# Kernel optimization log

Measured on AMD Instinct MI355X. Metric: run time of the kernel, lower is better.

The kernel has to match this reference:

```python
import jax, jax.numpy as jnp
import numpy as np

PATCH = 3  # match_patch_size

def _to_patches(fm, nph, npw):
    # fm: [1, C, H, W] -> [nph*npw, C*PATCH*PATCH] non-overlapping 3x3 patches
    C = fm.shape[1]
    x = fm[0, :, :nph * PATCH, :npw * PATCH].reshape(C, nph, PATCH, npw, PATCH)
    x = x.transpose(1, 3, 0, 2, 4)  # [nph, npw, C, p, p]
    return x.reshape(nph * npw, C * PATCH * PATCH)

def _from_patches(p, nph, npw, C):
    # [nph*npw, C*p*p] -> [1, C, nph*p, npw*p]
    x = p.reshape(nph, npw, C, PATCH, PATCH).transpose(2, 0, 3, 1, 4)
    return x.reshape(1, C, nph * PATCH, npw * PATCH)

def setup_inputs() -> dict:
    key = jax.random.key(0)
    k1, k2, k3 = jax.random.split(key, 3)
    C, H, W = 512, 252, 252
    style_fm = jax.random.normal(k1, (1, C, H, W), dtype=jnp.float32)
    img_fm = jax.random.normal(k2, (1, C, H, W), dtype=jnp.float32)
    mask = jax.random.uniform(k3, (1, 1, H, W), dtype=jnp.float32)
    return {"style_fm": style_fm, "img_fm": img_fm, "mask": mask}

def reference(style_fm, img_fm, mask):
    B, C, H, W = style_fm.shape  # B == 1
    nph, npw = H // PATCH, W // PATCH
    # Patch match: each img patch is a conv kernel applied to style_fm with
    # stride=PATCH -> score positions == non-overlapping style patch grid.
    img_p = _to_patches(img_fm, nph, npw)      # [P, D]
    sty_p = _to_patches(style_fm, nph, npw)    # [Q, D]
    scores = img_p @ sty_p.T                   # [P, Q] cross-correlation
    idx = jnp.argmax(scores, axis=1)           # best style patch per img patch
    matched = sty_p[idx]                       # [P, D] gather
    matched_fm = _from_patches(matched, nph, npw, C)
    style_matched = style_fm.at[:, :, :nph * PATCH, :npw * PATCH].set(matched_fm)
    # Mask (expanded as in capture_content), then Gram / sum(expanded mask)
    masked = style_matched * mask
    mask_sum = jnp.sum(jnp.broadcast_to(mask, style_matched.shape))
    gram = jnp.einsum('bchw,bdhw->bcd', masked, masked) / mask_sum  # [1, C, C]
    return gram
```

## Files before the change

### kernel.cpp

```cpp
#include <hip/hip_runtime.h>
#include <stdint.h>

typedef _Float16 f16;
typedef _Float16 f16x8 __attribute__((ext_vector_type(8)));
typedef float f32x4 __attribute__((ext_vector_type(4)));

#define NCH   512
#define IMH   252
#define IMW   252
#define HWSZ  (IMH*IMW)
#define NP    84
#define PN    (NP*NP)
#define PPAD  7168
#define DD    (NCH*9)
#define KK2   (PPAD*9)
#define KSPLIT 48
#define KCH   (KK2/KSPLIT)
#define MARGIN 1.0f

#define AS1(p) ((const __attribute__((address_space(1))) void*)(p))
#define AS3(p) ((__attribute__((address_space(3))) void*)(p))

__global__ void k_init(f16* __restrict__ I, f16* __restrict__ S,
                       int* cnt, float* msum) {
  unsigned t = blockIdx.x * blockDim.x + threadIdx.x;
  if (t == 0) { *cnt = 0; *msum = 0.0f; }
  const unsigned padN = (PPAD - PN) * DD;
  for (unsigned i = t; i < padN; i += gridDim.x * blockDim.x) {
    I[(size_t)PN * DD + i] = (f16)0.0f;
    S[(size_t)PN * DD + i] = (f16)0.0f;
  }
}

__global__ void k_masksum(const float* __restrict__ mask, float* msum) {
  __shared__ float red[256];
  float s = 0.f;
  for (unsigned i = blockIdx.x * 256 + threadIdx.x; i < HWSZ; i += gridDim.x * 256)
    s += mask[i];
  red[threadIdx.x] = s; __syncthreads();
  for (int st = 128; st > 0; st >>= 1) {
    if ((int)threadIdx.x < st) red[threadIdx.x] += red[threadIdx.x + st];
    __syncthreads();
  }
  if (threadIdx.x == 0) atomicAdd(msum, red[0]);
}

__global__ __launch_bounds__(256)
void k_pack(const float* __restrict__ fm, f16* __restrict__ out) {
  __shared__ f16 T[32 * 756];
  const int py = blockIdx.x >> 4, cg = blockIdx.x & 15;
  const int c0 = cg * 32;
  for (int e = threadIdx.x; e < 32 * 756; e += 256) {
    int cc = e / 756, rx = e - cc * 756;
    T[e] = (f16)fm[(size_t)(c0 + cc) * HWSZ +
                   (size_t)(py * 3 + rx / 252) * IMW + (rx % 252)];
  }
  __syncthreads();
  for (int v = threadIdx.x; v < 84 * 36; v += 256) {
    int pxi = v / 36, d0 = (v - pxi * 36) * 8;
    f16x8 o;
#pragma unroll
    for (int k = 0; k < 8; ++k) {
      int d = d0 + k, cc = d / 9, j = d - cc * 9;
      o[k] = T[cc * 756 + (j / 3) * 252 + pxi * 3 + (j % 3)];
    }
    *(f16x8*)(out + (size_t)(py * NP + pxi) * DD + c0 * 9 + d0) = o;
  }
}

__global__ __launch_bounds__(512, 2)
void k_gemm256(const f16* __restrict__ A, const f16* __restrict__ B,
               f16* __restrict__ out) {
  __shared__ f16 Al[4][256][32];
  __shared__ f16 Bl[4][256][32];
  const int tid = threadIdx.x, w = tid >> 6, l = tid & 63;
  int bid = blockIdx.x;
  bid = (bid & 7) * 98 + (bid >> 3);
  const int bx = bid % 28, by = bid / 28;
  const size_t row0 = (size_t)by * 256, col0 = (size_t)bx * 256;
  const int wm = w >> 2, wn = w & 3;
  f32x4 acc[8][4] = {};
  const int srow = w * 16 + (l >> 2);
  const int scol = (l & 3) * 8;
  const f16* gA0 = A + (row0 + srow) * DD + scol;
  const f16* gA1 = A + (row0 + srow + 128) * DD + scol;
  const f16* gB0 = B + (col0 + srow) * DD + scol;
  const f16* gB1 = B + (col0 + srow + 128) * DD + scol;
  const int ldst = w * 512 + l * 8;
#define STG(tt, bb) do {                                                        \
    __builtin_amdgcn_global_load_lds(AS1(gA0 + (tt)*32), AS3(&Al[bb][0][0] + ldst),        16, 0, 0); \
    __builtin_amdgcn_global_load_lds(AS1(gA1 + (tt)*32), AS3(&Al[bb][0][0] + 4096 + ldst), 16, 0, 0); \
    __builtin_amdgcn_global_load_lds(AS1(gB0 + (tt)*32), AS3(&Bl[bb][0][0] + ldst),        16, 0, 0); \
    __builtin_amdgcn_global_load_lds(AS1(gB1 + (tt)*32), AS3(&Bl[bb][0][0] + 4096 + ldst), 16, 0, 0); \
  } while (0)
  STG(0, 0); STG(1, 1); STG(2, 2);
  const int fr = l & 15, kb = (l >> 4) * 8;
  const int NT = DD / 32;
  for (int t = 0; t < NT; ++t) {
    const int ts = (t + 3 < NT) ? t + 3 : NT - 1;
    const int bb = t & 3;
    STG(ts, (t + 3) & 3);
    asm volatile("s_waitcnt vmcnt(12)" ::: "memory");
    __builtin_amdgcn_s_barrier();
    __builtin_amdgcn_sched_barrier(0);
    f16x8 af[8], bf[4];
#pragma unroll
    for (int i = 0; i < 8; ++i) af[i] = *(const f16x8*)&Al[bb][wm * 128 + i * 16 + fr][kb];
#pragma unroll
    for (int j = 0; j < 4; ++j) bf[j] = *(const f16x8*)&Bl[bb][wn * 64 + j * 16 + fr][kb];
#pragma unroll
    for (int i = 0; i < 8; ++i)
#pragma unroll
      for (int j = 0; j < 4; ++j)
        acc[i][j] = __builtin_amdgcn_mfma_f32_16x16x32_f16(af[i], bf[j], acc[i][j], 0, 0, 0);
    asm volatile("s_waitcnt lgkmcnt(0)" ::: "memory");
    __builtin_amdgcn_sched_barrier(0);
    __builtin_amdgcn_s_barrier();
  }
#undef STG
  const int fq = l >> 4;
  const size_t orow = row0 + wm * 128, ocol = col0 + wn * 64;
#pragma unroll
  for (int i = 0; i < 8; ++i)
#pragma unroll
    for (int j = 0; j < 4; ++j)
#pragma unroll
      for (int r = 0; r < 4; ++r)
        out[(orow + i * 16 + fq * 4 + r) * PPAD + (ocol + j * 16 + fr)] =
            (f16)acc[i][j][r];
}

__global__ void k_top2(const f16* __restrict__ sc, int* __restrict__ idx,
                       float* __restrict__ max1v, int* __restrict__ amb, int* cnt) {
  const int p = blockIdx.x;
  const f16x8* row8 = (const f16x8*)(sc + (size_t)p * PPAD);
  float m1 = -1e30f, m2 = -1e30f; int i1 = 0;
  for (int v = threadIdx.x; v < PN / 8; v += 256) {
    f16x8 x = row8[v];
#pragma unroll
    for (int k = 0; k < 8; ++k) {
      float val = (float)x[k];
      if (val > m1) { m2 = m1; m1 = val; i1 = v * 8 + k; }
      else if (val > m2) m2 = val;
    }
  }
  __shared__ float sm1[256], sm2[256]; __shared__ int si1[256];
  const int t = threadIdx.x;
  sm1[t] = m1; sm2[t] = m2; si1[t] = i1; __syncthreads();
  for (int st = 128; st > 0; st >>= 1) {
    if (t < st) {
      float am1 = sm1[t], am2 = sm2[t]; int ai1 = si1[t];
      float bm1 = sm1[t + st], bm2 = sm2[t + st]; int bi1 = si1[t + st];
      if (bm1 > am1 || (bm1 == am1 && bi1 < ai1)) {
        sm1[t] = bm1; si1[t] = bi1; sm2[t] = fmaxf(am1, bm2);
      } else {
        sm2[t] = fmaxf(bm1, am2);
      }
    }
    __syncthreads();
  }
  if (t == 0) {
    idx[p] = si1[0]; max1v[p] = sm1[0];
    if (sm2[0] > sm1[0] - MARGIN) { int a = atomicAdd(cnt, 1); amb[a] = p; }
  }
}

__global__ void k_rescore(const float* __restrict__ img, const float* __restrict__ sty,
                          const f16* __restrict__ sc, const float* __restrict__ max1v,
                          const int* __restrict__ amb, const int* __restrict__ cnt,
                          int* __restrict__ idx) {
  __shared__ float red[256];
  __shared__ unsigned long long ball[4];
  const int t = threadIdx.x;
  const int n = *cnt;
  for (int r = blockIdx.x; r < n; r += gridDim.x) {
    const int p = amb[r];
    const float thr = max1v[p] - MARGIN;
    const f16* row = sc + (size_t)p * PPAD;
    const int py = (p / NP) * 3, px = (p % NP) * 3;
    float best = -1e30f; int bq = 0x7fffffff;
    for (int base = 0; base < PN; base += 256) {
      const int q = base + t;
      const bool is_cand = (q < PN) && ((float)row[q] >= thr);
      unsigned long long m = __ballot(is_cand);
      if ((t & 63) == 0) ball[t >> 6] = m;
      __syncthreads();
      for (int wv = 0; wv < 4; ++wv) {
        unsigned long long mm = ball[wv];
        while (mm) {
          const int b = __ffsll(mm) - 1; mm &= mm - 1;
          const int q2 = base + wv * 64 + b;
          const int qy = (q2 / NP) * 3, qx = (q2 % NP) * 3;
          float s = 0.f;
          for (int d = t; d < DD; d += 256) {
            int c = d / 9, j = d - c * 9, dy = j / 3, dx = j - dy * 3;
            s += img[(size_t)c * HWSZ + (py + dy) * IMW + (px + dx)] *
                 sty[(size_t)c * HWSZ + (qy + dy) * IMW + (qx + dx)];
          }
          red[t] = s; __syncthreads();
          for (int st = 128; st > 0; st >>= 1) {
            if (t < st) red[t] += red[t + st];
            __syncthreads();
          }
          const float tot = red[0];
          __syncthreads();
          if (tot > best || (tot == best && q2 < bq)) { best = tot; bq = q2; }
        }
      }
      __syncthreads();
    }
    if (t == 0) idx[p] = bq;
    __syncthreads();
  }
}

__global__ __launch_bounds__(256)
void k_masked(const f16* __restrict__ S, const int* __restrict__ idx,
              const float* __restrict__ mask, f16* __restrict__ M) {
  __shared__ f16 B[84 * 288];
  __shared__ float mrow[756];
  __shared__ int qv[84];
  const int py = blockIdx.x >> 4, cg = blockIdx.x & 15;
  const int c0 = cg * 32;
  for (int e = threadIdx.x; e < 756; e += 256)
    mrow[e] = mask[(size_t)(py * 3 + e / 252) * IMW + (e % 252)];
  if (threadIdx.x < 84) qv[threadIdx.x] = idx[py * NP + threadIdx.x];
  __syncthreads();
  for (int v = threadIdx.x; v < 84 * 36; v += 256) {
    int pxi = v / 36, d0 = (v - pxi * 36) * 8;
    f16x8 x = *(const f16x8*)(S + (size_t)qv[pxi] * DD + c0 * 9 + d0);
    f16x8 o;
#pragma unroll
    for (int k = 0; k < 8; ++k) {
      int j = (d0 + k) % 9;
      o[k] = (f16)((float)x[k] * mrow[(j / 3) * 252 + pxi * 3 + (j % 3)]);
    }
    *(f16x8*)(&B[pxi * 288 + d0]) = o;
  }
  __syncthreads();
  for (int e = threadIdx.x; e < 32 * 756; e += 256) {
    int cc = e / 756, r = e - cc * 756;
    M[(size_t)(c0 + cc) * KK2 + (size_t)py * 756 + r] =
        B[(r / 9) * 288 + cc * 9 + (r % 9)];
  }
}

__global__ void k_mpad(f16* __restrict__ M) {
  const unsigned per_c = (PPAD - PN) * 9;
  const unsigned total = NCH * per_c;
  for (unsigned e = blockIdx.x * 256 + threadIdx.x; e < total;
       e += gridDim.x * 256) {
    unsigned c = e / per_c, r = e - c * per_c;
    M[(size_t)c * KK2 + (size_t)PN * 9 + r] = (f16)0.0f;
  }
}

__global__ __launch_bounds__(256, 3)
void k_gram(const f16* __restrict__ M, float* __restrict__ part) {
  __shared__ f16 As[128][32];
  __shared__ f16 Bs[128][32];
  const int tid = threadIdx.x;
  const int w = tid >> 6, l = tid & 63;
  const int tile = blockIdx.x & 15, chunk = blockIdx.x >> 4;
  const int bx = tile & 3, by = tile >> 2;
  const size_t row0 = (size_t)by * 128, col0 = (size_t)bx * 128;
  const int wr = w >> 1, wc = w & 1;
  f32x4 acc[4][4] = {};
  const int sr = w * 32 + (l >> 2);
  const int skb = (l & 3) * 8;
  const int kbeg = chunk * KCH;
  const f16* ga = M + (row0 + sr) * KK2 + kbeg + skb;
  const f16* gb = M + (col0 + sr) * KK2 + kbeg + skb;
  f16* lA0 = &As[w * 32][0];  f16* lA1 = &As[w * 32 + 16][0];
  f16* lB0 = &Bs[w * 32][0];  f16* lB1 = &Bs[w * 32 + 16][0];
  const int fr = l & 15, kb = (l >> 4) * 8;
  for (int k0 = 0; k0 < KCH; k0 += 32) {
    __syncthreads();
    __builtin_amdgcn_global_load_lds(AS1(ga),            AS3(lA0), 16, 0, 0);
    __builtin_amdgcn_global_load_lds(AS1(ga + 16 * KK2), AS3(lA1), 16, 0, 0);
    __builtin_amdgcn_global_load_lds(AS1(gb),            AS3(lB0), 16, 0, 0);
    __builtin_amdgcn_global_load_lds(AS1(gb + 16 * KK2), AS3(lB1), 16, 0, 0);
    ga += 32; gb += 32;
    asm volatile("s_waitcnt vmcnt(0)" ::: "memory");
    __syncthreads();
    f16x8 af[4], bf[4];
#pragma unroll
    for (int i = 0; i < 4; ++i) af[i] = *(const f16x8*)&As[wr * 64 + i * 16 + fr][kb];
#pragma unroll
    for (int j = 0; j < 4; ++j) bf[j] = *(const f16x8*)&Bs[wc * 64 + j * 16 + fr][kb];
#pragma unroll
    for (int i = 0; i < 4; ++i)
#pragma unroll
      for (int j = 0; j < 4; ++j)
        acc[i][j] = __builtin_amdgcn_mfma_f32_16x16x32_f16(af[i], bf[j], acc[i][j], 0, 0, 0);
  }
  const int fq = l >> 4;
  const size_t orow = row0 + wr * 64, ocol = col0 + wc * 64;
  float* pout = part + (size_t)chunk * (NCH * NCH);
#pragma unroll
  for (int i = 0; i < 4; ++i)
#pragma unroll
    for (int j = 0; j < 4; ++j)
#pragma unroll
      for (int r = 0; r < 4; ++r)
        pout[(orow + i * 16 + fq * 4 + r) * NCH + (ocol + j * 16 + fr)] = acc[i][j][r];
}

__global__ void k_out(const float* __restrict__ part, const float* __restrict__ msum,
                      float* __restrict__ out) {
  const unsigned e = blockIdx.x * 256 + threadIdx.x;
  float s = 0.f;
#pragma unroll
  for (int k = 0; k < KSPLIT; ++k) s += part[(size_t)k * (NCH * NCH) + e];
  out[e] = s / (*msum * (float)NCH);
}

extern "C" void kernel_launch(void* const* d_in, const int* in_sizes, int n_in,
                              void* d_out, int out_size, void* d_ws, size_t ws_size,
                              hipStream_t stream) {
  const float* style = (const float*)d_in[0];
  const float* img   = (const float*)d_in[1];
  const float* mask  = (const float*)d_in[2];
  float* out = (float*)d_out;
  char* ws = (char*)d_ws;

  const size_t SZP = (size_t)PPAD * DD * sizeof(f16);
  const size_t SZS = (size_t)PPAD * PPAD * sizeof(f16);
  f16* I  = (f16*)(ws);
  f16* S  = (f16*)(ws + SZP);
  f16* SC = (f16*)(ws + 2 * SZP);
  char* misc = ws + 2 * SZP + SZS;
  int*   idx   = (int*)(misc);
  float* max1v = (float*)(misc + 32768);
  int*   amb   = (int*)(misc + 65536);
  int*   cnt   = (int*)(misc + 98304);
  float* msum  = (float*)(misc + 98432);
  float* part  = (float*)(ws);

  k_init   <<<256, 256, 0, stream>>>(I, S, cnt, msum);
  k_masksum<<<128, 256, 0, stream>>>(mask, msum);
  k_pack   <<<84 * 16, 256, 0, stream>>>(img, I);
  k_pack   <<<84 * 16, 256, 0, stream>>>(style, S);
  k_gemm256<<<(PPAD / 256) * (PPAD / 256), 512, 0, stream>>>(I, S, SC);
  k_top2   <<<PN, 256, 0, stream>>>(SC, idx, max1v, amb, cnt);
  k_rescore<<<512, 256, 0, stream>>>(img, style, SC, max1v, amb, cnt, idx);
  k_masked <<<84 * 16, 256, 0, stream>>>(S, idx, mask, SC);
  k_mpad   <<<128, 256, 0, stream>>>(SC);
  k_gram   <<<16 * KSPLIT, 256, 0, stream>>>((const f16*)SC, part);
  k_out    <<<(NCH * NCH) / 256, 256, 0, stream>>>(part, msum, out);
}
```

Measured before the change: 1.316 ms.

## Shrink score GEMM tile to 128x128 and XOR-swizzle LDS in GEMM and Gram

The main score GEMM goes from 256x256 tiles with 512 threads to 128x128 tiles with 256 threads, so there are four times as many workgroups and each holds fewer accumulators. Both the score GEMM and the Gram kernel now XOR-swizzle the k-offset of global-to-LDS loads and the matching fragment reads, meant to reduce LDS bank conflicts on the MFMA operand reads. In exchange, the smaller tiles reuse each loaded operand less, so the large score GEMM moves more global and L2 traffic.

```diff
diff --git a/kernel.cpp b/kernel.cpp
--- a/kernel.cpp
+++ b/kernel.cpp
@@ -21,6 +21,7 @@
 #define AS1(p) ((const __attribute__((address_space(1))) void*)(p))
 #define AS3(p) ((__attribute__((address_space(3))) void*)(p))
 
+
 __global__ void k_init(f16* __restrict__ I, f16* __restrict__ S,
                        int* cnt, float* msum) {
   unsigned t = blockIdx.x * blockDim.x + threadIdx.x;
@@ -68,33 +69,34 @@
   }
 }
 
-__global__ __launch_bounds__(512, 2)
-void k_gemm256(const f16* __restrict__ A, const f16* __restrict__ B,
-               f16* __restrict__ out) {
-  __shared__ f16 Al[4][256][32];
-  __shared__ f16 Bl[4][256][32];
+__global__ __launch_bounds__(256, 2)
+void k_gemm(const f16* __restrict__ A, const f16* __restrict__ B,
+            f16* __restrict__ out) {
+  __shared__ f16 Al[4][128][32];
+  __shared__ f16 Bl[4][128][32];
   const int tid = threadIdx.x, w = tid >> 6, l = tid & 63;
+  const int nwg = (PPAD / 128) * (PPAD / 128);
   int bid = blockIdx.x;
-  bid = (bid & 7) * 98 + (bid >> 3);
-  const int bx = bid % 28, by = bid / 28;
-  const size_t row0 = (size_t)by * 256, col0 = (size_t)bx * 256;
-  const int wm = w >> 2, wn = w & 3;
-  f32x4 acc[8][4] = {};
-  const int srow = w * 16 + (l >> 2);
-  const int scol = (l & 3) * 8;
-  const f16* gA0 = A + (row0 + srow) * DD + scol;
-  const f16* gA1 = A + (row0 + srow + 128) * DD + scol;
-  const f16* gB0 = B + (col0 + srow) * DD + scol;
-  const f16* gB1 = B + (col0 + srow + 128) * DD + scol;
-  const int ldst = w * 512 + l * 8;
-#define STG(tt, bb) do {                                                        \
-    __builtin_amdgcn_global_load_lds(AS1(gA0 + (tt)*32), AS3(&Al[bb][0][0] + ldst),        16, 0, 0); \
-    __builtin_amdgcn_global_load_lds(AS1(gA1 + (tt)*32), AS3(&Al[bb][0][0] + 4096 + ldst), 16, 0, 0); \
-    __builtin_amdgcn_global_load_lds(AS1(gB0 + (tt)*32), AS3(&Bl[bb][0][0] + ldst),        16, 0, 0); \
-    __builtin_amdgcn_global_load_lds(AS1(gB1 + (tt)*32), AS3(&Bl[bb][0][0] + 4096 + ldst), 16, 0, 0); \
+  bid = (bid & 7) * (nwg >> 3) + (bid >> 3);
+  const int bx = bid % (PPAD / 128), by = bid / (PPAD / 128);
+  const size_t row0 = (size_t)by * 128, col0 = (size_t)bx * 128;
+  const int wr = w >> 1, wc = w & 1;
+  f32x4 acc[4][4] = {};
+  const int sr = w * 32 + (l >> 2);
+  const int ssw = ((l & 3) ^ ((l >> 2) & 3)) * 8;
+  const f16* gA0 = A + (row0 + sr) * DD + ssw;
+  const f16* gA1 = gA0 + 16 * DD;
+  const f16* gB0 = B + (col0 + sr) * DD + ssw;
+  const f16* gB1 = gB0 + 16 * DD;
+#define STG(tt, bb) do {                                                                   \
+    __builtin_amdgcn_global_load_lds(AS1(gA0 + (tt)*32), AS3(&Al[bb][w*32][0]      + l*8), 16, 0, 0); \
+    __builtin_amdgcn_global_load_lds(AS1(gA1 + (tt)*32), AS3(&Al[bb][w*32+16][0]   + l*8), 16, 0, 0); \
+    __builtin_amdgcn_global_load_lds(AS1(gB0 + (tt)*32), AS3(&Bl[bb][w*32][0]      + l*8), 16, 0, 0); \
+    __builtin_amdgcn_global_load_lds(AS1(gB1 + (tt)*32), AS3(&Bl[bb][w*32+16][0]   + l*8), 16, 0, 0); \
   } while (0)
   STG(0, 0); STG(1, 1); STG(2, 2);
-  const int fr = l & 15, kb = (l >> 4) * 8;
+  const int fr = l & 15;
+  const int swk = ((l >> 4) ^ (l & 3)) * 8;
   const int NT = DD / 32;
   for (int t = 0; t < NT; ++t) {
     const int ts = (t + 3 < NT) ? t + 3 : NT - 1;
@@ -103,13 +105,13 @@
     asm volatile("s_waitcnt vmcnt(12)" ::: "memory");
     __builtin_amdgcn_s_barrier();
     __builtin_amdgcn_sched_barrier(0);
-    f16x8 af[8], bf[4];
-#pragma unroll
-    for (int i = 0; i < 8; ++i) af[i] = *(const f16x8*)&Al[bb][wm * 128 + i * 16 + fr][kb];
-#pragma unroll
-    for (int j = 0; j < 4; ++j) bf[j] = *(const f16x8*)&Bl[bb][wn * 64 + j * 16 + fr][kb];
-#pragma unroll
-    for (int i = 0; i < 8; ++i)
+    f16x8 af[4], bf[4];
+#pragma unroll
+    for (int i = 0; i < 4; ++i) af[i] = *(const f16x8*)&Al[bb][wr * 64 + i * 16 + fr][swk];
+#pragma unroll
+    for (int j = 0; j < 4; ++j) bf[j] = *(const f16x8*)&Bl[bb][wc * 64 + j * 16 + fr][swk];
+#pragma unroll
+    for (int i = 0; i < 4; ++i)
 #pragma unroll
       for (int j = 0; j < 4; ++j)
         acc[i][j] = __builtin_amdgcn_mfma_f32_16x16x32_f16(af[i], bf[j], acc[i][j], 0, 0, 0);
@@ -119,9 +121,9 @@
   }
 #undef STG
   const int fq = l >> 4;
-  const size_t orow = row0 + wm * 128, ocol = col0 + wn * 64;
-#pragma unroll
-  for (int i = 0; i < 8; ++i)
+  const size_t orow = row0 + wr * 64, ocol = col0 + wc * 64;
+#pragma unroll
+  for (int i = 0; i < 4; ++i)
 #pragma unroll
     for (int j = 0; j < 4; ++j)
 #pragma unroll
@@ -267,27 +269,28 @@
   const int wr = w >> 1, wc = w & 1;
   f32x4 acc[4][4] = {};
   const int sr = w * 32 + (l >> 2);
-  const int skb = (l & 3) * 8;
+  const int ssw = ((l & 3) ^ ((l >> 2) & 3)) * 8;
   const int kbeg = chunk * KCH;
-  const f16* ga = M + (row0 + sr) * KK2 + kbeg + skb;
-  const f16* gb = M + (col0 + sr) * KK2 + kbeg + skb;
+  const f16* ga = M + (row0 + sr) * KK2 + kbeg + ssw;
+  const f16* gb = M + (col0 + sr) * KK2 + kbeg + ssw;
   f16* lA0 = &As[w * 32][0];  f16* lA1 = &As[w * 32 + 16][0];
   f16* lB0 = &Bs[w * 32][0];  f16* lB1 = &Bs[w * 32 + 16][0];
-  const int fr = l & 15, kb = (l >> 4) * 8;
+  const int fr = l & 15;
+  const int swk = ((l >> 4) ^ (l & 3)) * 8;
   for (int k0 = 0; k0 < KCH; k0 += 32) {
     __syncthreads();
-    __builtin_amdgcn_global_load_lds(AS1(ga),            AS3(lA0), 16, 0, 0);
-    __builtin_amdgcn_global_load_lds(AS1(ga + 16 * KK2), AS3(lA1), 16, 0, 0);
-    __builtin_amdgcn_global_load_lds(AS1(gb),            AS3(lB0), 16, 0, 0);
-    __builtin_amdgcn_global_load_lds(AS1(gb + 16 * KK2), AS3(lB1), 16, 0, 0);
+    __builtin_amdgcn_global_load_lds(AS1(ga),            AS3(lA0 + l * 8), 16, 0, 0);
+    __builtin_amdgcn_global_load_lds(AS1(ga + 16 * KK2), AS3(lA1 + l * 8), 16, 0, 0);
+    __builtin_amdgcn_global_load_lds(AS1(gb),            AS3(lB0 + l * 8), 16, 0, 0);
+    __builtin_amdgcn_global_load_lds(AS1(gb + 16 * KK2), AS3(lB1 + l * 8), 16, 0, 0);
     ga += 32; gb += 32;
     asm volatile("s_waitcnt vmcnt(0)" ::: "memory");
     __syncthreads();
     f16x8 af[4], bf[4];
 #pragma unroll
-    for (int i = 0; i < 4; ++i) af[i] = *(const f16x8*)&As[wr * 64 + i * 16 + fr][kb];
-#pragma unroll
-    for (int j = 0; j < 4; ++j) bf[j] = *(const f16x8*)&Bs[wc * 64 + j * 16 + fr][kb];
+    for (int i = 0; i < 4; ++i) af[i] = *(const f16x8*)&As[wr * 64 + i * 16 + fr][swk];
+#pragma unroll
+    for (int j = 0; j < 4; ++j) bf[j] = *(const f16x8*)&Bs[wc * 64 + j * 16 + fr][swk];
 #pragma unroll
     for (int i = 0; i < 4; ++i)
 #pragma unroll
@@ -341,7 +344,7 @@
   k_masksum<<<128, 256, 0, stream>>>(mask, msum);
   k_pack   <<<84 * 16, 256, 0, stream>>>(img, I);
   k_pack   <<<84 * 16, 256, 0, stream>>>(style, S);
-  k_gemm256<<<(PPAD / 256) * (PPAD / 256), 512, 0, stream>>>(I, S, SC);
+  k_gemm   <<<(PPAD / 128) * (PPAD / 128), 256, 0, stream>>>(I, S, SC);
   k_top2   <<<PN, 256, 0, stream>>>(SC, idx, max1v, amb, cnt);
   k_rescore<<<512, 256, 0, stream>>>(img, style, SC, max1v, amb, cnt, idx);
   k_masked <<<84 * 16, 256, 0, stream>>>(S, idx, mask, SC);
```

Result: no change. 1.318 ms (+0.1%).
